# Kernel tuning notes

Measured on AMD Instinct MI355X. Metric: run time of the kernel, lower is better.

The kernel has to match this reference:

```python
import jax, jax.numpy as jnp
import numpy as np


def _tconv(X, W, b):
    # X: [B, N, T, Cin], W: [1, K, Cin, Cout] -> [B, N, T-K+1, Cout]
    y = jax.lax.conv_general_dilated(
        X, W, window_strides=(1, 1), padding='VALID',
        dimension_numbers=('NHWC', 'HWIO', 'NHWC'))
    return y + b


def _timeblock(X, W, b):
    # W: [3, 1, K, Cin, Cout], b: [3, Cout]
    temp = _tconv(X, W[0], b[0]) + _tconv(X, W[1], b[1])
    gate = jax.nn.sigmoid(_tconv(X, W[2], b[2]))
    return jax.nn.relu(gate * temp)


def _stgcn_block(X, A_hat, Wa, ba, theta, Wb, bb):
    t = _timeblock(X, Wa, ba)                         # [B, N, T', 64]
    lfs = jnp.einsum('ij,bjtm->bitm', A_hat, t)       # graph aggregation
    t2 = jax.nn.relu(jnp.einsum('bitm,mp->bitp', lfs, theta))
    return _timeblock(t2, Wb, bb)


def setup_inputs() -> dict:
    key = jax.random.key(0)
    ks = jax.random.split(key, 20)
    B, N, T, C = 16, 2048, 24, 2
    s = 0.1
    A = jax.random.uniform(ks[1], (N, N), dtype=jnp.float32)
    A = A / jnp.sum(A, axis=1, keepdims=True)  # row-normalized adjacency
    return {
        'x': jax.random.normal(ks[0], (B, N, T, C), dtype=jnp.float32),
        'A_hat': A,
        'tb1_w': jax.random.normal(ks[2], (3, 1, 3, 2, 64), dtype=jnp.float32) * s,
        'tb1_b': jax.random.normal(ks[3], (3, 64), dtype=jnp.float32) * s,
        'theta1': jax.random.normal(ks[4], (64, 16), dtype=jnp.float32) * s,
        'tb2_w': jax.random.normal(ks[5], (3, 1, 3, 16, 64), dtype=jnp.float32) * s,
        'tb2_b': jax.random.normal(ks[6], (3, 64), dtype=jnp.float32) * s,
        'tb3_w': jax.random.normal(ks[7], (3, 1, 3, 64, 64), dtype=jnp.float32) * s,
        'tb3_b': jax.random.normal(ks[8], (3, 64), dtype=jnp.float32) * s,
        'theta2': jax.random.normal(ks[9], (64, 16), dtype=jnp.float32) * s,
        'tb4_w': jax.random.normal(ks[10], (3, 1, 3, 16, 64), dtype=jnp.float32) * s,
        'tb4_b': jax.random.normal(ks[11], (3, 64), dtype=jnp.float32) * s,
        'tb5_w': jax.random.normal(ks[12], (3, 1, 3, 64, 64), dtype=jnp.float32) * s,
        'tb5_b': jax.random.normal(ks[13], (3, 64), dtype=jnp.float32) * s,
        'fully_w': jax.random.normal(ks[14], (896, 12), dtype=jnp.float32) * s,
        'fully_b': jax.random.normal(ks[15], (12,), dtype=jnp.float32) * s,
    }


def reference(x, A_hat, tb1_w, tb1_b, theta1, tb2_w, tb2_b,
              tb3_w, tb3_b, theta2, tb4_w, tb4_b,
              tb5_w, tb5_b, fully_w, fully_b):
    out1 = _stgcn_block(x, A_hat, tb1_w, tb1_b, theta1, tb2_w, tb2_b)
    out2 = _stgcn_block(out1, A_hat, tb3_w, tb3_b, theta2, tb4_w, tb4_b)
    out3 = _timeblock(out2, tb5_w, tb5_b)             # [B, N, T-10, 64]
    B, N = out3.shape[0], out3.shape[1]
    out4 = out3.reshape(B, N, -1) @ fully_w + fully_b  # [B, N, pred_num]
    return (out4, A_hat)
```

## Files before the change

kernel.cpp:

```cpp
#include <hip/hip_runtime.h>

typedef unsigned short u16;
typedef unsigned int u32;
typedef __attribute__((ext_vector_type(4))) float f32x4;
typedef __attribute__((ext_vector_type(8))) short s16x8;

__device__ __forceinline__ u16 f2bf(float f) {
  union { float f; u32 u; } v; v.f = f;
  u32 u = v.u;
  return (u16)((u + 0x7fffu + ((u >> 16) & 1u)) >> 16);
}
__device__ __forceinline__ float bf2f(u16 b) {
  union { u32 u; float f; } v; v.u = ((u32)b) << 16;
  return v.f;
}
__device__ __forceinline__ float sigmoidf(float x) {
  return __builtin_amdgcn_rcpf(1.0f + __expf(-x));
}

__device__ __forceinline__ void async16(const void* g, void* l) {
  __builtin_amdgcn_global_load_lds(
      (const __attribute__((address_space(1))) u32*)g,
      (__attribute__((address_space(3))) u32*)l, 16, 0, 0);
}

__device__ __forceinline__ u32 pk_bf16(float lo, float hi) {
  u32 r;
  asm("v_cvt_pk_bf16_f32 %0, %1, %2" : "=v"(r) : "v"(lo), "v"(hi));
  return r;
}

__device__ __forceinline__ void prep_w_body(
    const float* __restrict__ tw, u16* __restrict__ WcT,
    int CIN, int WK, int idx)
{
  if (idx >= 128 * WK) return;
  const int c = idx / WK;
  const int k = idx - c * WK;
  const int KR = CIN * 3;
  float v = 0.0f;
  if (k < KR) {
    const int k3 = k / CIN, cin = k - k3 * CIN;
    if (c < 64)
      v = tw[(k3 * CIN + cin) * 64 + c] + tw[(3 * CIN + k3 * CIN + cin) * 64 + c];
    else
      v = tw[(6 * CIN + k3 * CIN + cin) * 64 + (c - 64)];
  }
  WcT[idx] = f2bf(v);
}

__global__ __launch_bounds__(256) void prep_all(
    const float* __restrict__ A, u16* __restrict__ Abf, float* __restrict__ outA,
    const float* __restrict__ tb1w, u16* __restrict__ W1,
    const float* __restrict__ tb2w, u16* __restrict__ W2,
    const float* __restrict__ tb3w, u16* __restrict__ W3,
    const float* __restrict__ tb4w, u16* __restrict__ W4,
    const float* __restrict__ tb5w, u16* __restrict__ W5,
    const float* __restrict__ fw, u16* __restrict__ FWT)
{
  const int bx = blockIdx.x;
  const int tid = threadIdx.x;
  if (bx < 4096) {
    const long i = ((long)bx * 256 + tid) * 4;
    float4 v = *(const float4*)(A + i);
    *(float4*)(outA + i) = v;
    ushort4 p;
    p.x = f2bf(v.x); p.y = f2bf(v.y); p.z = f2bf(v.z); p.w = f2bf(v.w);
    *(ushort4*)(Abf + i) = p;
  } else if (bx < 4100) {
    prep_w_body(tb1w, W1, 2, 8, (bx - 4096) * 256 + tid);
  } else if (bx < 4132) {
    prep_w_body(tb2w, W2, 16, 64, (bx - 4100) * 256 + tid);
  } else if (bx < 4228) {
    prep_w_body(tb3w, W3, 64, 192, (bx - 4132) * 256 + tid);
  } else if (bx < 4260) {
    prep_w_body(tb4w, W4, 16, 64, (bx - 4228) * 256 + tid);
  } else if (bx < 4356) {
    prep_w_body(tb5w, W5, 64, 192, (bx - 4260) * 256 + tid);
  } else {
    const int idx = (bx - 4356) * 256 + tid;
    if (idx < 16 * 896) {
      const int p = idx / 896, k = idx - p * 896;
      FWT[idx] = f2bf(p < 12 ? fw[k * 12 + p] : 0.0f);
    }
  }
}

__global__ __launch_bounds__(256) void tb1_kernel(
    const float* __restrict__ x, const u16* __restrict__ W1,
    const float* __restrict__ bias, const float* __restrict__ th1,
    u16* __restrict__ U1)
{
  __shared__ float Bts[64], Bgs[64];
  __shared__ u16 t2buf[4][16 * 64];
  const int tid = threadIdx.x;
  if (tid < 64) { Bts[tid] = bias[tid] + bias[64 + tid]; Bgs[tid] = bias[128 + tid]; }
  const int lane = tid & 63, w = tid >> 6;
  const int lm = lane & 15, q = lane >> 4;
  const int b = blockIdx.y, t = blockIdx.z;
  const int n0 = blockIdx.x * 256 + w * 64;

  s16x8 wfrag[8];
#pragma unroll
  for (int mt = 0; mt < 8; mt++) {
    wfrag[mt] = (s16x8){0, 0, 0, 0, 0, 0, 0, 0};
    if (q == 0) wfrag[mt] = *(const s16x8*)(W1 + (mt * 16 + lm) * 8);
  }
  s16x8 tfrag[2];
#pragma unroll
  for (int kk = 0; kk < 2; kk++)
#pragma unroll
    for (int j = 0; j < 8; j++)
      tfrag[kk][j] = (short)f2bf(th1[(kk * 32 + q * 8 + j) * 16 + lm]);

  float xv[4][6];
  if (q == 0) {
#pragma unroll
    for (int nt = 0; nt < 4; nt++) {
      const float* xp = x + ((long)(b * 2048 + n0 + nt * 16 + lm) * 24 + t) * 2;
#pragma unroll
      for (int j = 0; j < 6; j++) xv[nt][j] = xp[j];
    }
  }
  __syncthreads();
  float bt4[4][4], bg4[4][4];
#pragma unroll
  for (int mt = 0; mt < 4; mt++)
#pragma unroll
    for (int r = 0; r < 4; r++) {
      bt4[mt][r] = Bts[mt * 16 + q * 4 + r];
      bg4[mt][r] = Bgs[mt * 16 + q * 4 + r];
    }

  u16* myt2 = t2buf[w];
  const long orowbase = (long)((b * 22 + t) * 16) << 11;

#pragma unroll
  for (int nt = 0; nt < 4; nt++) {
    s16x8 pfrag = (s16x8){0, 0, 0, 0, 0, 0, 0, 0};
    if (q == 0) {
#pragma unroll
      for (int j = 0; j < 6; j++) pfrag[j] = (short)f2bf(xv[nt][j]);
    }
    f32x4 acc1[8];
#pragma unroll
    for (int mt = 0; mt < 8; mt++) acc1[mt] = f32x4{0.f, 0.f, 0.f, 0.f};
#pragma unroll
    for (int mt = 0; mt < 8; mt++)
      acc1[mt] = __builtin_amdgcn_mfma_f32_16x16x32_bf16(wfrag[mt], pfrag, acc1[mt], 0, 0, 0);

#pragma unroll
    for (int mt = 0; mt < 4; mt++) {
      u32 pk[2];
      u16 pv[4];
#pragma unroll
      for (int r = 0; r < 4; r++) {
        const float temp = acc1[mt][r] + bt4[mt][r];
        const float ga = acc1[mt + 4][r] + bg4[mt][r];
        pv[r] = f2bf(fmaxf(temp * sigmoidf(ga), 0.0f));
      }
      pk[0] = (u32)pv[0] | ((u32)pv[1] << 16);
      pk[1] = (u32)pv[2] | ((u32)pv[3] << 16);
      const int g = (mt * 4 + q) >> 1, half = q & 1;
      *(uint2*)(myt2 + lm * 64 + (g ^ (lm & 7)) * 8 + half * 4) = make_uint2(pk[0], pk[1]);
    }

    f32x4 acc2 = f32x4{0.f, 0.f, 0.f, 0.f};
#pragma unroll
    for (int kk = 0; kk < 2; kk++) {
      s16x8 af = *(const s16x8*)(myt2 + lm * 64 + ((kk * 4 + q) ^ (lm & 7)) * 8);
      acc2 = __builtin_amdgcn_mfma_f32_16x16x32_bf16(af, tfrag[kk], acc2, 0, 0, 0);
    }
    u16 ov[4];
#pragma unroll
    for (int r = 0; r < 4; r++) ov[r] = f2bf(acc2[r]);
    *(uint2*)(U1 + orowbase + ((long)lm << 11) + n0 + nt * 16 + q * 4) =
        make_uint2((u32)ov[0] | ((u32)ov[1] << 16), (u32)ov[2] | ((u32)ov[3] << 16));
  }
}

template <int RELU>
__global__ __launch_bounds__(256, 3) void sp_gemm(
    const u16* __restrict__ A, const u16* __restrict__ X,
    u16* __restrict__ C, int Ncols, int nwg)
{
  __shared__ u16 ldsA[128 * 64];
  __shared__ u16 ldsB[128 * 64];
  const int lane = threadIdx.x & 63;
  const int w = threadIdx.x >> 6;

  const int h = blockIdx.x;
  const int bx = (h & 7) * (nwg >> 3) + (h >> 3);

  const int ct = bx >> 4;
  const int rt = bx & 15;
  const int i0 = rt * 128;
  const int c0 = ct * 128;

  const int wm = w & 1, wn = w >> 1;
  const int lm = lane & 15, q = lane >> 4;

  f32x4 acc[4][4];
#pragma unroll
  for (int a = 0; a < 4; a++)
#pragma unroll
    for (int b2 = 0; b2 < 4; b2++) acc[a][b2] = f32x4{0.f, 0.f, 0.f, 0.f};

  const int srow = lane >> 3;
  const int sg = (lane & 7) ^ srow;
  const u16* gA = A + ((long)(i0 + w * 32 + srow) << 11) + sg * 8;
  const u16* gB = X + ((long)(c0 + w * 32 + srow) << 11) + sg * 8;
  u16* lA = ldsA + w * 2048;
  u16* lB = ldsB + w * 2048;

  for (int k0 = 0; k0 < 2048; k0 += 64) {
    __syncthreads();
#pragma unroll
    for (int j = 0; j < 4; j++) {
      async16(gA + j * 16384 + k0, lA + j * 512);
      async16(gB + j * 16384 + k0, lB + j * 512);
    }
    __syncthreads();
#pragma unroll
    for (int kk = 0; kk < 2; kk++) {
      const int ph = (kk * 4 + q) ^ (lm & 7);
      s16x8 af[4], bfr[4];
#pragma unroll
      for (int mt = 0; mt < 4; mt++)
        af[mt] = *(const s16x8*)(ldsA + (wm * 64 + mt * 16 + lm) * 64 + ph * 8);
#pragma unroll
      for (int nt = 0; nt < 4; nt++)
        bfr[nt] = *(const s16x8*)(ldsB + (wn * 64 + nt * 16 + lm) * 64 + ph * 8);
#pragma unroll
      for (int mt = 0; mt < 4; mt++)
#pragma unroll
        for (int nt = 0; nt < 4; nt++)
          acc[mt][nt] = __builtin_amdgcn_mfma_f32_16x16x32_bf16(af[mt], bfr[nt], acc[mt][nt], 0, 0, 0);
    }
  }

#pragma unroll
  for (int mt = 0; mt < 4; mt++) {
#pragma unroll
    for (int r = 0; r < 4; r++) {
      const long i = i0 + wm * 64 + mt * 16 + q * 4 + r;
      u16* crow = C + i * Ncols + c0 + wn * 64 + lm;
#pragma unroll
      for (int nt = 0; nt < 4; nt++) {
        float v = acc[mt][nt][r];
        if (RELU) v = fmaxf(v, 0.0f);
        crow[nt * 16] = f2bf(v);
      }
    }
  }
}

template <int TIN, int MODE>
__global__ __launch_bounds__(256, 2) void tbf_fused(
    const u16* __restrict__ in, const u16* __restrict__ W1c,
    const float* __restrict__ b1, const u16* __restrict__ W2c,
    const float* __restrict__ b2, const float* __restrict__ th,
    const u16* __restrict__ fwT, const float* __restrict__ fb,
    u16* __restrict__ outU, float* __restrict__ outF)
{
  constexpr int T1OUT = TIN - 2;
  constexpr int T2OUT = TIN - 4;
  constexpr int NC = TIN * 256;

  __shared__ __align__(16) u16 ring[8 * 1024];
  __shared__ __align__(16) u16 h2r[3 * 64 * 64];
  __shared__ __align__(16) u16 h3b[64 * 64];
  __shared__ __align__(16) u16 sfw[(MODE == 0) ? 12 * 904 : 8];

  const int tid = threadIdx.x;
  const int lane = tid & 63;
  const int w = tid >> 6;
  const int lm = lane & 15, q = lane >> 4;
  const int bx = blockIdx.x;
  const int n0 = (bx & 31) << 6;
  const int b = bx >> 5;

  s16x8 wfA[2][2];
  {
    const u16* wp = W1c + (w * 16 + lm) * 64 + q * 8;
#pragma unroll
    for (int kk = 0; kk < 2; kk++) {
      wfA[0][kk] = *(const s16x8*)(wp + kk * 32);
      wfA[1][kk] = *(const s16x8*)(wp + 64 * 64 + kk * 32);
    }
  }
  s16x8 wfB[2][6];
  {
    const u16* wp = W2c + (w * 16 + lm) * 192 + q * 8;
#pragma unroll
    for (int kk = 0; kk < 6; kk++) {
      wfB[0][kk] = *(const s16x8*)(wp + kk * 32);
      wfB[1][kk] = *(const s16x8*)(wp + 64 * 192 + kk * 32);
    }
  }
  const int cw = w * 16 + q * 4;
  float bsA4[4], bgA4[4], bsB4[4], bgB4[4];
#pragma unroll
  for (int r = 0; r < 4; r++) {
    bsA4[r] = b1[cw + r] + b1[64 + cw + r];
    bgA4[r] = b1[128 + cw + r];
    bsB4[r] = b2[cw + r] + b2[64 + cw + r];
    bgB4[r] = b2[128 + cw + r];
  }

  s16x8 tfrag[2];
  const int srow12 = (lm < 12) ? lm : (lm - 12);
  if constexpr (MODE == 1) {
#pragma unroll
    for (int kk = 0; kk < 2; kk++)
#pragma unroll
      for (int j = 0; j < 8; j++)
        tfrag[kk][j] = (short)f2bf(th[(kk * 32 + q * 8 + j) * 16 + lm]);
  } else {
#pragma unroll
    for (int i = 0; i < 6; i++) {
      const int g = i * 256 + tid;
      if (g < 12 * 112) {
        const int p = g / 112, k8 = g - p * 112;
        *(s16x8*)(sfw + p * 904 + k8 * 8) = *(const s16x8*)(fwT + g * 8);
      }
    }
  }
  asm volatile("" : "+v"(bsA4[0]), "+v"(bsA4[1]), "+v"(bsA4[2]), "+v"(bsA4[3]),
                    "+v"(bgA4[0]), "+v"(bgA4[1]), "+v"(bgA4[2]), "+v"(bgA4[3]),
                    "+v"(bsB4[0]), "+v"(bsB4[1]), "+v"(bsB4[2]), "+v"(bsB4[3]),
                    "+v"(bgB4[0]), "+v"(bgB4[1]), "+v"(bgB4[2]), "+v"(bgB4[3]));
  asm volatile("s_waitcnt vmcnt(0)" ::: "memory");

  const int k7 = tid & 127;
  const int segsel = tid >> 7;
  const u16* rowp = in + (long)(n0 + (k7 >> 1)) * NC + (long)(b * TIN) * 16 + (k7 & 1) * 8;

  auto issue_pair = [&](int tp) {
    const int seg = tp + segsel;
    async16(rowp + seg * 16, ring + ((seg & 7) << 10) + k7 * 8);
  };

  issue_pair(0); issue_pair(2); issue_pair(4);

  u16* h2w = h2r;
  u16* h2m = h2r + 64 * 64;
  u16* h2o = h2r + 2 * 64 * 64;
  f32x4 accfc = f32x4{0.f, 0.f, 0.f, 0.f};

  const int gw8 = 2 * w + (q >> 1);
  const int wofs = (q & 1) << 2;

#pragma unroll 1
  for (int t = 0; t < T1OUT; ++t) {
    if constexpr (MODE == 1) {
      if (t < 3) asm volatile("s_waitcnt vmcnt(1) lgkmcnt(0)" ::: "memory");
      else       asm volatile("s_waitcnt vmcnt(2) lgkmcnt(0)" ::: "memory");
    } else {
      if (t < 13) asm volatile("s_waitcnt vmcnt(1) lgkmcnt(0)" ::: "memory");
      else        asm volatile("s_waitcnt vmcnt(0) lgkmcnt(0)" ::: "memory");
    }
    __builtin_amdgcn_s_barrier();

    if (((t & 1) == 0) && t <= TIN - 8) issue_pair(t + 6);

    {
      f32x4 aA[4][2];
#pragma unroll
      for (int m = 0; m < 4; m++) {
        aA[m][0] = f32x4{0.f, 0.f, 0.f, 0.f};
        aA[m][1] = f32x4{0.f, 0.f, 0.f, 0.f};
      }
#pragma unroll
      for (int kk = 0; kk < 2; kk++) {
        const int slotb = ((t + 2 * kk + (q >> 1)) & 7) << 10;
        const int off = slotb + (q & 1) * 8;
#pragma unroll
        for (int nt = 0; nt < 4; nt++) {
          s16x8 pf = *(const s16x8*)(ring + off + (nt * 16 + lm) * 16);
          aA[nt][0] = __builtin_amdgcn_mfma_f32_16x16x32_bf16(wfA[0][kk], pf, aA[nt][0], 0, 0, 0);
          aA[nt][1] = __builtin_amdgcn_mfma_f32_16x16x32_bf16(wfA[1][kk], pf, aA[nt][1], 0, 0, 0);
        }
      }
#pragma unroll
      for (int nt = 0; nt < 4; nt++) {
        float hv[4];
#pragma unroll
        for (int r = 0; r < 4; r++) {
          const float temp = aA[nt][0][r] + bsA4[r];
          const float ga = aA[nt][1][r] + bgA4[r];
          hv[r] = fmaxf(temp * sigmoidf(ga), 0.0f);
        }
        *(uint2*)(h2w + ((nt * 16 + lm) << 6) + ((gw8 ^ (lm & 7)) << 3) + wofs) =
            make_uint2(pk_bf16(hv[0], hv[1]), pk_bf16(hv[2], hv[3]));
      }
    }
    asm volatile("s_waitcnt lgkmcnt(0)" ::: "memory");
    __builtin_amdgcn_s_barrier();

    if (t >= 2) {
      f32x4 aB[4][2];
#pragma unroll
      for (int m = 0; m < 4; m++) {
        aB[m][0] = f32x4{0.f, 0.f, 0.f, 0.f};
        aB[m][1] = f32x4{0.f, 0.f, 0.f, 0.f};
      }
#pragma unroll
      for (int kk3 = 0; kk3 < 6; kk3++) {
        const u16* hp = (kk3 < 2) ? h2o : ((kk3 < 4) ? h2m : h2w);
        const int gr = (kk3 & 1) * 4 + q;
#pragma unroll
        for (int nt = 0; nt < 4; nt++) {
          s16x8 pf = *(const s16x8*)(hp + ((nt * 16 + lm) << 6) + ((gr ^ (lm & 7)) << 3));
          aB[nt][0] = __builtin_amdgcn_mfma_f32_16x16x32_bf16(wfB[0][kk3], pf, aB[nt][0], 0, 0, 0);
          aB[nt][1] = __builtin_amdgcn_mfma_f32_16x16x32_bf16(wfB[1][kk3], pf, aB[nt][1], 0, 0, 0);
        }
      }
#pragma unroll
      for (int nt = 0; nt < 4; nt++) {
        float hv[4];
#pragma unroll
        for (int r = 0; r < 4; r++) {
          const float temp = aB[nt][0][r] + bsB4[r];
          const float ga = aB[nt][1][r] + bgB4[r];
          hv[r] = fmaxf(temp * sigmoidf(ga), 0.0f);
        }
        *(uint2*)(h3b + ((nt * 16 + lm) << 6) + ((gw8 ^ (lm & 7)) << 3) + wofs) =
            make_uint2(pk_bf16(hv[0], hv[1]), pk_bf16(hv[2], hv[3]));
      }
      asm volatile("s_waitcnt lgkmcnt(0)" ::: "memory");
      __builtin_amdgcn_s_barrier();

      const int t2 = t - 2;
      if constexpr (MODE == 1) {
        f32x4 a4 = f32x4{0.f, 0.f, 0.f, 0.f};
#pragma unroll
        for (int kk = 0; kk < 2; kk++) {
          s16x8 af = *(const s16x8*)(h3b + ((w * 16 + lm) << 6) + (((kk * 4 + q) ^ (lm & 7)) << 3));
          a4 = __builtin_amdgcn_mfma_f32_16x16x32_bf16(af, tfrag[kk], a4, 0, 0, 0);
        }
        u16 ov[4];
#pragma unroll
        for (int r = 0; r < 4; r++) ov[r] = f2bf(a4[r]);
        const long orowbase = (long)((b * T2OUT + t2) * 16) << 11;
        *(uint2*)(outU + orowbase + ((long)lm << 11) + n0 + w * 16 + q * 4) =
            make_uint2((u32)ov[0] | ((u32)ov[1] << 16), (u32)ov[2] | ((u32)ov[3] << 16));
      } else {
#pragma unroll
        for (int kk = 0; kk < 2; kk++) {
          s16x8 af = *(const s16x8*)(h3b + ((w * 16 + lm) << 6) + (((kk * 4 + q) ^ (lm & 7)) << 3));
          s16x8 bfr = *(const s16x8*)(sfw + srow12 * 904 + t2 * 64 + kk * 32 + q * 8);
          accfc = __builtin_amdgcn_mfma_f32_16x16x32_bf16(af, bfr, accfc, 0, 0, 0);
        }
      }
    }
    u16* tmp = h2o; h2o = h2m; h2m = h2w; h2w = tmp;
  }

  if constexpr (MODE == 0) {
    if (lm < 12) {
      const float bfc = fb[lm];
#pragma unroll
      for (int r = 0; r < 4; r++) {
        const int n = n0 + w * 16 + q * 4 + r;
        outF[((long)b * 2048 + n) * 12 + lm] = accfc[r] + bfc;
      }
    }
  }
}

extern "C" void kernel_launch(void* const* d_in, const int* in_sizes, int n_in,
                              void* d_out, int out_size, void* d_ws, size_t ws_size,
                              hipStream_t stream)
{
  const float* x    = (const float*)d_in[0];
  const float* A    = (const float*)d_in[1];
  const float* tb1w = (const float*)d_in[2];
  const float* tb1b = (const float*)d_in[3];
  const float* th1  = (const float*)d_in[4];
  const float* tb2w = (const float*)d_in[5];
  const float* tb2b = (const float*)d_in[6];
  const float* tb3w = (const float*)d_in[7];
  const float* tb3b = (const float*)d_in[8];
  const float* th2  = (const float*)d_in[9];
  const float* tb4w = (const float*)d_in[10];
  const float* tb4b = (const float*)d_in[11];
  const float* tb5w = (const float*)d_in[12];
  const float* tb5b = (const float*)d_in[13];
  const float* fw   = (const float*)d_in[14];
  const float* fb   = (const float*)d_in[15];
  float* out = (float*)d_out;

  char* ws = (char*)d_ws;
  u16* Abf  = (u16*)(ws + 0);
  u16* W2   = (u16*)(ws + 8388608);
  u16* W3   = (u16*)(ws + 8404992);
  u16* W4   = (u16*)(ws + 8454144);
  u16* W5   = (u16*)(ws + 8470528);
  u16* bufA = (u16*)(ws + 8519680);
  u16* bufB = (u16*)(ws + 100794368);
  u16* W1   = (u16*)(ws + 8519680 + 88000000);
  u16* FWT  = (u16*)(ws + 8519680 + 88004096);

  prep_all<<<4412, 256, 0, stream>>>(A, Abf, out + 393216,
                                     tb1w, W1, tb2w, W2, tb3w, W3,
                                     tb4w, W4, tb5w, W5, fw, FWT);

  tb1_kernel<<<dim3(8, 16, 22), 256, 0, stream>>>(x, W1, tb1b, th1, bufA);
  sp_gemm<1><<<44 * 16, 256, 0, stream>>>(Abf, bufA, bufB, 5632, 44 * 16);
  tbf_fused<22, 1><<<512, 256, 0, stream>>>(bufB, W2, tb2b, W3, tb3b, th2,
                                            nullptr, nullptr, bufA, nullptr);
  sp_gemm<1><<<36 * 16, 256, 0, stream>>>(Abf, bufA, bufB, 4608, 36 * 16);
  tbf_fused<18, 0><<<512, 256, 0, stream>>>(bufB, W4, tb4b, W5, tb5b, nullptr,
                                            FWT, fb, nullptr, out);
}
```

Baseline: 310.1 us.

## Split MODE 1 fused timeblock kernel along time into two halves

The first fused timeblock kernel (TIN=22) now launches 1024 blocks instead of 512, and each block handles half of the output time steps with a start offset t0. Each half recomputes two overlapping halo steps of the first temporal conv. Loads past the end of the input are clamped to the last valid time step. The aim is to fill more CUs and raise occupancy on the MI355X, at the cost of some redundant compute and weight/bias loading per block.

New measurement: 322.9 us. 1.04x slower.

```diff
diff --git a/kernel.cpp b/kernel.cpp
--- a/kernel.cpp
+++ b/kernel.cpp
@@ -263,9 +263,12 @@
     const u16* __restrict__ fwT, const float* __restrict__ fb,
     u16* __restrict__ outU, float* __restrict__ outF)
 {
-  constexpr int T1OUT = TIN - 2;
   constexpr int T2OUT = TIN - 4;
   constexpr int NC = TIN * 256;
+  constexpr int NSP = (MODE == 1) ? 2 : 1;
+  constexpr int T2H = T2OUT / NSP;
+  constexpr int NI  = T2H + 2;
+  constexpr int JISS = (MODE == 1) ? 6 : 10;
 
   __shared__ __align__(16) u16 ring[8 * 1024];
   __shared__ __align__(16) u16 h2r[3 * 64 * 64];
@@ -278,7 +281,8 @@
   const int lm = lane & 15, q = lane >> 4;
   const int bx = blockIdx.x;
   const int n0 = (bx & 31) << 6;
-  const int b = bx >> 5;
+  const int b = (bx >> 5) & 15;
+  const int t0 = (MODE == 1) ? ((bx >> 9) * T2H) : 0;
 
   s16x8 wfA[2][2];
   {
@@ -338,10 +342,12 @@
 
   auto issue_pair = [&](int tp) {
     const int seg = tp + segsel;
-    async16(rowp + seg * 16, ring + ((seg & 7) << 10) + k7 * 8);
+    const int sega = (seg < TIN) ? seg : (TIN - 1);
+    async16(rowp + sega * 16,
+            ring + ((seg & 7) << 10) + k7 * 8);
   };
 
-  issue_pair(0); issue_pair(2); issue_pair(4);
+  issue_pair(t0); issue_pair(t0 + 2); issue_pair(t0 + 4);
 
   u16* h2w = h2r;
   u16* h2m = h2r + 64 * 64;
@@ -352,17 +358,18 @@
   const int wofs = (q & 1) << 2;
 
 #pragma unroll 1
-  for (int t = 0; t < T1OUT; ++t) {
+  for (int j = 0; j < NI; ++j) {
+    const int t = t0 + j;
     if constexpr (MODE == 1) {
-      if (t < 3) asm volatile("s_waitcnt vmcnt(1) lgkmcnt(0)" ::: "memory");
+      if (j < 3) asm volatile("s_waitcnt vmcnt(1) lgkmcnt(0)" ::: "memory");
       else       asm volatile("s_waitcnt vmcnt(2) lgkmcnt(0)" ::: "memory");
     } else {
-      if (t < 13) asm volatile("s_waitcnt vmcnt(1) lgkmcnt(0)" ::: "memory");
+      if (j < 13) asm volatile("s_waitcnt vmcnt(1) lgkmcnt(0)" ::: "memory");
       else        asm volatile("s_waitcnt vmcnt(0) lgkmcnt(0)" ::: "memory");
     }
     __builtin_amdgcn_s_barrier();
 
-    if (((t & 1) == 0) && t <= TIN - 8) issue_pair(t + 6);
+    if (((j & 1) == 0) && j <= JISS) issue_pair(t + 6);
 
     {
       f32x4 aA[4][2];
@@ -398,7 +405,7 @@
     asm volatile("s_waitcnt lgkmcnt(0)" ::: "memory");
     __builtin_amdgcn_s_barrier();
 
-    if (t >= 2) {
+    if (j >= 2) {
       f32x4 aB[4][2];
 #pragma unroll
       for (int m = 0; m < 4; m++) {
@@ -431,7 +438,7 @@
       asm volatile("s_waitcnt lgkmcnt(0)" ::: "memory");
       __builtin_amdgcn_s_barrier();
 
-      const int t2 = t - 2;
+      const int o2 = t - 2;
       if constexpr (MODE == 1) {
         f32x4 a4 = f32x4{0.f, 0.f, 0.f, 0.f};
 #pragma unroll
@@ -442,14 +449,14 @@
         u16 ov[4];
 #pragma unroll
         for (int r = 0; r < 4; r++) ov[r] = f2bf(a4[r]);
-        const long orowbase = (long)((b * T2OUT + t2) * 16) << 11;
+        const long orowbase = (long)((b * T2OUT + o2) * 16) << 11;
         *(uint2*)(outU + orowbase + ((long)lm << 11) + n0 + w * 16 + q * 4) =
             make_uint2((u32)ov[0] | ((u32)ov[1] << 16), (u32)ov[2] | ((u32)ov[3] << 16));
       } else {
 #pragma unroll
         for (int kk = 0; kk < 2; kk++) {
           s16x8 af = *(const s16x8*)(h3b + ((w * 16 + lm) << 6) + (((kk * 4 + q) ^ (lm & 7)) << 3));
-          s16x8 bfr = *(const s16x8*)(sfw + srow12 * 904 + t2 * 64 + kk * 32 + q * 8);
+          s16x8 bfr = *(const s16x8*)(sfw + srow12 * 904 + o2 * 64 + kk * 32 + q * 8);
           accfc = __builtin_amdgcn_mfma_f32_16x16x32_bf16(af, bfr, accfc, 0, 0, 0);
         }
       }
@@ -508,8 +515,8 @@
 
   tb1_kernel<<<dim3(8, 16, 22), 256, 0, stream>>>(x, W1, tb1b, th1, bufA);
   sp_gemm<1><<<44 * 16, 256, 0, stream>>>(Abf, bufA, bufB, 5632, 44 * 16);
-  tbf_fused<22, 1><<<512, 256, 0, stream>>>(bufB, W2, tb2b, W3, tb3b, th2,
-                                            nullptr, nullptr, bufA, nullptr);
+  tbf_fused<22, 1><<<1024, 256, 0, stream>>>(bufB, W2, tb2b, W3, tb3b, th2,
+                                             nullptr, nullptr, bufA, nullptr);
   sp_gemm<1><<<36 * 16, 256, 0, stream>>>(Abf, bufA, bufB, 4608, 36 * 16);
   tbf_fused<18, 0><<<512, 256, 0, stream>>>(bufB, W4, tb4b, W5, tb5b, nullptr,
                                             FWT, fb, nullptr, out);
```
